# Performance work log

Hardware: AMD Instinct MI355X
Metric: run time of the kernel (lower is better)

## Reference

```python
import jax, jax.numpy as jnp
import numpy as np
from jax import lax

MARGIN = 0.3
BIGF = 1e9


def _pairwise_dist(x):
    # dist[i,j] = ||x_i - x_j||, clamped at 1e-12 before sqrt (as in torch code)
    sq = jnp.sum(x * x, axis=1)
    d = sq[:, None] + sq[None, :] - 2.0 * (x @ x.T)
    return jnp.sqrt(jnp.clip(d, 1e-12))


def _hard_mining(dist, targets):
    is_pos = targets[:, None] == targets[None, :]
    ap = jnp.where(is_pos, dist, jnp.asarray(-BIGF, dist.dtype))
    an = jnp.where(is_pos, jnp.asarray(BIGF, dist.dtype), dist)
    dist_ap = jnp.max(ap, axis=1)
    p_inds = jnp.argmax(ap, axis=1)
    dist_an = jnp.min(an, axis=1)
    n_inds = jnp.argmin(an, axis=1)
    return dist_ap, dist_an, p_inds, n_inds


def _batch_euclidean(x, y):
    # x: [N,m,d], y: [N,n,d] -> [N,m,n]
    xx = jnp.sum(x * x, axis=-1)[:, :, None]
    yy = jnp.sum(y * y, axis=-1)[:, None, :]
    d = xx + yy - 2.0 * jnp.einsum('nmd,nkd->nmk', x, y)
    return jnp.sqrt(jnp.clip(d, 1e-12))


def _shortest_dist(dmat):
    # DTW-style shortest path over [m,n] grid, batched over N: dp[i,j] = d[i,j] + min(dp[i-1,j], dp[i,j-1])
    N, m, n = dmat.shape
    big = jnp.asarray(BIGF, dmat.dtype)
    init_row = jnp.full((N, n), big, dmat.dtype).at[:, 0].set(0.0)  # virtual row -1: only (0,0) reachable

    def row_step(prev_row, drow):  # prev_row,drow: [N,n]
        def col_step(left, un):  # left: [N]
            up, d = un
            cur = d + jnp.minimum(up, left)
            return cur, cur
        _, cols = lax.scan(col_step, jnp.full((N,), big, dmat.dtype), (prev_row.T, drow.T))
        return cols.T, None

    last_row, _ = lax.scan(row_step, init_row, jnp.moveaxis(dmat, 1, 0))
    return last_row[:, -1]


def _batch_local_dist(x, y):
    d = _batch_euclidean(x, y)
    d = jnp.tanh(d * 0.5)  # == (exp(d)-1)/(exp(d)+1), numerically safe
    return _shortest_dist(d)


def _margin_ranking(dist_an, dist_ap, margin):
    # MarginRankingLoss with y=1: mean(relu(margin - (dist_an - dist_ap)))
    return jnp.mean(jnp.maximum(0.0, margin + dist_ap - dist_an))


def setup_inputs() -> dict:
    key = jax.random.key(0)
    k1, k2 = jax.random.split(key)
    N, D = 512, 2048
    LD, PARTS = 128, 8
    K = 4  # instances per identity (PK sampling)
    inputs = jax.random.normal(k1, (N, D), dtype=jnp.float32)
    local_features = jax.random.normal(k2, (N, LD, PARTS), dtype=jnp.float32)
    targets = jnp.arange(N, dtype=jnp.int64) // K
    return {"inputs": inputs, "targets": targets, "local_features": local_features}


def reference(inputs, targets, local_features):
    dist = _pairwise_dist(inputs)
    dist_ap, dist_an, p_inds, n_inds = _hard_mining(dist, targets)
    global_loss = _margin_ranking(dist_an, dist_ap, MARGIN)
    lf = jnp.transpose(local_features, (0, 2, 1))  # [N, parts, local_dim]
    local_ap = _batch_local_dist(lf, lf[p_inds])
    local_an = _batch_local_dist(lf, lf[n_inds])
    local_loss = _margin_ranking(local_an, local_ap, MARGIN)
    return (global_loss, local_loss)
```

## Files before the change

### kernel.cpp

```cpp
#include <hip/hip_runtime.h>
#include <math.h>

#define MARGIN 0.3f
#define BIGF 1e9f
#define NN 512
#define DD 2048
#define LDIM 128
#define PARTS 8

typedef __attribute__((ext_vector_type(8))) __bf16 bf16x8;
typedef __attribute__((ext_vector_type(4))) float f32x4;

__global__ __launch_bounds__(256, 2) void k_gram(
    const float* __restrict__ X, _Float16* __restrict__ Gp,
    float* __restrict__ ndiag, float* gsum, float* lsum, unsigned* counter)
{
    __shared__ __bf16 A[2][4096], B[2][4096];

    int bid = blockIdx.x;
    int tj = bid & 7, ti = (bid >> 3) & 7, ks = bid >> 6;
    int t = threadIdx.x;
    int w = t >> 6, lane = t & 63;
    int wr = w >> 1, wc = w & 1;

    if (bid == 0 && t == 0) { *gsum = 0.0f; *lsum = 0.0f; *counter = 0u; }

    int m = t >> 7;
    int r = (t >> 1) & 63;
    int kst = t & 1;
    int grow = (m ? tj : ti) * 64 + r;
    const float4* gp4 = (const float4*)(X + (size_t)grow * DD + ks * 256 + kst * 32);
    int ebase = kst * 2048 + (r >> 4) * 512 + (r & 15) * 8;

    float4 cur[8];
#pragma unroll
    for (int q = 0; q < 8; q++) cur[q] = gp4[q];

    f32x4 acc00 = {0.f, 0.f, 0.f, 0.f};
    f32x4 acc01 = {0.f, 0.f, 0.f, 0.f};
    f32x4 acc10 = {0.f, 0.f, 0.f, 0.f};
    f32x4 acc11 = {0.f, 0.f, 0.f, 0.f};

    {
        __bf16* hb = (m ? B[0] : A[0]) + ebase;
#pragma unroll
        for (int jg = 0; jg < 4; jg++) {
            float fe[8] = {cur[2 * jg].x, cur[2 * jg].y, cur[2 * jg].z, cur[2 * jg].w,
                           cur[2 * jg + 1].x, cur[2 * jg + 1].y, cur[2 * jg + 1].z, cur[2 * jg + 1].w};
            bf16x8 h;
#pragma unroll
            for (int e = 0; e < 8; e++) h[e] = (__bf16)fe[e];
            *(bf16x8*)(hb + jg * 128) = h;
        }
    }

#pragma unroll
    for (int it = 0; it < 4; ++it) {
        __syncthreads();
        if (it < 3) {
            const float4* np = gp4 + (it + 1) * 16;
#pragma unroll
            for (int q = 0; q < 8; q++) cur[q] = np[q];
        }
        int buf = it & 1;
#pragma unroll
        for (int kstep = 0; kstep < 2; kstep++) {
            const bf16x8* fA = (const bf16x8*)&A[buf][kstep * 2048 + wr * 1024];
            const bf16x8* fB = (const bf16x8*)&B[buf][kstep * 2048 + wc * 1024];
            bf16x8 ah0 = fA[lane], ah1 = fA[lane + 64];
            bf16x8 bh0 = fB[lane], bh1 = fB[lane + 64];
            acc00 = __builtin_amdgcn_mfma_f32_16x16x32_bf16(ah0, bh0, acc00, 0, 0, 0);
            acc01 = __builtin_amdgcn_mfma_f32_16x16x32_bf16(ah0, bh1, acc01, 0, 0, 0);
            acc10 = __builtin_amdgcn_mfma_f32_16x16x32_bf16(ah1, bh0, acc10, 0, 0, 0);
            acc11 = __builtin_amdgcn_mfma_f32_16x16x32_bf16(ah1, bh1, acc11, 0, 0, 0);
        }
        if (it < 3) {
            int nb = (it + 1) & 1;
            __bf16* hb = (m ? B[nb] : A[nb]) + ebase;
#pragma unroll
            for (int jg = 0; jg < 4; jg++) {
                float fe[8] = {cur[2 * jg].x, cur[2 * jg].y, cur[2 * jg].z, cur[2 * jg].w,
                               cur[2 * jg + 1].x, cur[2 * jg + 1].y, cur[2 * jg + 1].z, cur[2 * jg + 1].w};
                bf16x8 h;
#pragma unroll
                for (int e = 0; e < 8; e++) h[e] = (__bf16)fe[e];
                *(bf16x8*)(hb + jg * 128) = h;
            }
        }
    }

    int rbase = ti * 64 + wr * 32 + ((lane >> 4) << 2);
    int cbase = tj * 64 + wc * 32 + (lane & 15);
    _Float16* gb = Gp + (size_t)ks * NN * NN;
    f32x4 accs[2][2] = {{acc00, acc01}, {acc10, acc11}};
#pragma unroll
    for (int g = 0; g < 2; g++)
#pragma unroll
        for (int h = 0; h < 2; h++)
#pragma unroll
            for (int rr = 0; rr < 4; rr++)
                gb[(size_t)(rbase + g * 16 + rr) * NN + cbase + h * 16] =
                    (_Float16)accs[g][h][rr];

    if (ti == tj && wr == wc && ((lane >> 4) == ((lane & 15) >> 2))) {
        int rr = lane & 3;
        int row0 = rbase + rr;
        ndiag[ks * NN + row0]      = acc00[rr];
        ndiag[ks * NN + row0 + 16] = acc11[rr];
    }
}

__global__ __launch_bounds__(256) void k_mine_local(
    const _Float16* __restrict__ Gp, const float* __restrict__ ndiag,
    const int* __restrict__ tg, const float* __restrict__ LF,
    float* gsum, float* lsum, unsigned* counter, float* __restrict__ out)
{
    __shared__ float s_apv[4]; __shared__ int s_api[4];
    __shared__ float s_anv[4]; __shared__ int s_ani[4];
    __shared__ int sh_pn[2];
    __shared__ float A2[LDIM * PARTS];
    __shared__ float B2[2][LDIM * PARTS];
    __shared__ float dtm[2][64];
    __shared__ float res[2];

    int i = blockIdx.x;
    int t = threadIdx.x;

    float4 a2v = ((const float4*)(LF + (size_t)i * LDIM * PARTS))[t];

    float ni = 0.f, d0 = 0.f, d1 = 0.f;
#pragma unroll
    for (int ks = 0; ks < 8; ks++) {
        ni += ndiag[ks * NN + i];
        d0 += ndiag[ks * NN + t];
        d1 += ndiag[ks * NN + t + 256];
    }

    int tgt_i = tg[i];

    float apv = -BIGF; int api = 0x7fffffff;
    float anv =  BIGF; int ani = 0x7fffffff;

#pragma unroll
    for (int jj = 0; jj < 2; jj++) {
        int j = t + jj * 256;
        float g = 0.f;
#pragma unroll
        for (int ks = 0; ks < 8; ks++)
            g += (float)Gp[(size_t)ks * NN * NN + (size_t)i * NN + j];
        float nj = (jj == 0) ? d0 : d1;
        float dd = ni + nj - 2.0f * g;
        float dist = sqrtf(fmaxf(dd, 1e-12f));
        bool pos = (tg[j] == tgt_i);
        float a = pos ? dist : -BIGF;
        if (a > apv || (a == apv && j < api)) { apv = a; api = j; }
        float b = pos ? BIGF : dist;
        if (b < anv || (b == anv && j < ani)) { anv = b; ani = j; }
    }
    for (int off = 32; off > 0; off >>= 1) {
        float av = __shfl_down(apv, off); int ai = __shfl_down(api, off);
        if (av > apv || (av == apv && ai < api)) { apv = av; api = ai; }
        float nv = __shfl_down(anv, off); int nid = __shfl_down(ani, off);
        if (nv < anv || (nv == anv && nid < ani)) { anv = nv; ani = nid; }
    }
    int lane = t & 63, wid = t >> 6;
    if (lane == 0) { s_apv[wid] = apv; s_api[wid] = api;
                     s_anv[wid] = anv; s_ani[wid] = ani; }
    __syncthreads();
    if (t == 0) {
        apv = s_apv[0]; api = s_api[0]; anv = s_anv[0]; ani = s_ani[0];
        for (int wv = 1; wv < 4; wv++) {
            float av = s_apv[wv]; int ai = s_api[wv];
            if (av > apv || (av == apv && ai < api)) { apv = av; api = ai; }
            float nv = s_anv[wv]; int nid = s_ani[wv];
            if (nv < anv || (nv == anv && nid < ani)) { anv = nv; ani = nid; }
        }
        sh_pn[0] = api;
        sh_pn[1] = ani;
        atomicAdd(gsum, fmaxf(0.0f, MARGIN + apv - anv));
    }
    __syncthreads();

    int w = t >> 6;
    ((float4*)A2)[t] = a2v;
    if (w < 2) {
        int ind = sh_pn[w];
        const float4* B4 = (const float4*)(LF + (size_t)ind * LDIM * PARTS);
        float4* Bw = (float4*)B2[w];
        Bw[lane]       = B4[lane];
        Bw[lane + 64]  = B4[lane + 64];
        Bw[lane + 128] = B4[lane + 128];
        Bw[lane + 192] = B4[lane + 192];
    }
    __syncthreads();

    if (w < 2) {
        int p = lane >> 3, q = lane & 7;
        float acc = 0.0f;
        const float* Bw = B2[w];
        for (int d = 0; d < LDIM; d++) {
            float diff = A2[d * PARTS + p] - Bw[d * PARTS + q];
            acc = fmaf(diff, diff, acc);
        }
        float dist = sqrtf(fmaxf(acc, 1e-12f));
        dtm[w][p * 8 + q] = tanhf(0.5f * dist);
    }
    __syncthreads();

    if ((t == 0) || (t == 64)) {
        const float* dm = dtm[w];
        float dp[8];
        dp[0] = dm[0];
        for (int j = 1; j < 8; j++) dp[j] = dp[j - 1] + dm[j];
        for (int rr = 1; rr < 8; rr++) {
            dp[0] += dm[rr * 8];
            for (int j = 1; j < 8; j++)
                dp[j] = dm[rr * 8 + j] + fminf(dp[j], dp[j - 1]);
        }
        res[w] = dp[7];
    }
    __syncthreads();

    if (t == 0) {
        float l = fmaxf(0.0f, MARGIN + res[0] - res[1]);
        atomicAdd(lsum, l);
        __threadfence();
        unsigned old = atomicAdd(counter, 1u);
        if (old == (NN - 1)) {
            __threadfence();
            float ls = atomicAdd(lsum, 0.0f);
            float gs = atomicAdd(gsum, 0.0f);
            out[0] = gs * (1.0f / NN);
            out[1] = ls * (1.0f / NN);
        }
    }
}

extern "C" void kernel_launch(void* const* d_in, const int* in_sizes, int n_in,
                              void* d_out, int out_size, void* d_ws, size_t ws_size,
                              hipStream_t stream)
{
    const float* X  = (const float*)d_in[0];
    const int*   tg = (const int*)d_in[1];
    const float* LF = (const float*)d_in[2];
    float* out = (float*)d_out;

    char* ws = (char*)d_ws;
    _Float16* Gp      = (_Float16*)ws;
    float*    ndiag   = (float*)(ws + (4u << 20));
    float*    gsum    = (float*)(ws + (4u << 20) + 16384);
    float*    lsum    = (float*)(ws + (4u << 20) + 16388);
    unsigned* counter = (unsigned*)(ws + (4u << 20) + 16392);

    k_gram<<<512, 256, 0, stream>>>(X, Gp, ndiag, gsum, lsum, counter);
    k_mine_local<<<512, 256, 0, stream>>>(Gp, ndiag, tg, LF, gsum, lsum, counter, out);
}
```

Measured before the change: 94.25 us.

## Fuse Gram and mining kernels into one persistent kernel with grid barrier

Merges the split-K Gram kernel and the mining/local-distance kernel into a single launch. A global atomic counter acts as a grid-wide barrier, the two phases share LDS through a union, and diagonal norms are accumulated atomically into one array. The mining phase also reads two fp16 partials per thread as one 32-bit load. This removes a kernel launch and the gap between the two launches, but adds a hipMemsetAsync and a spin barrier that relies on all 512 blocks being co-resident, which risks deadlock if occupancy does not allow it.

```diff
diff --git a/kernel.cpp b/kernel.cpp
--- a/kernel.cpp
+++ b/kernel.cpp
@@ -11,72 +11,54 @@
 typedef __attribute__((ext_vector_type(8))) __bf16 bf16x8;
 typedef __attribute__((ext_vector_type(4))) float f32x4;
 
-__global__ __launch_bounds__(256, 2) void k_gram(
-    const float* __restrict__ X, _Float16* __restrict__ Gp,
-    float* __restrict__ ndiag, float* gsum, float* lsum, unsigned* counter)
+union SMem {
+  struct { __bf16 A[2][4096]; __bf16 B[2][4096]; } g;
+  struct {
+    float A2[LDIM * PARTS];
+    float B2[2][LDIM * PARTS];
+    float dtm[2][64];
+    float res[2];
+    float apv[4]; float anv[4];
+    int   api[4]; int   ani[4];
+    int   pn[2];
+  } m;
+};
+
+__global__ __launch_bounds__(256, 2) void k_fused(
+    const float* __restrict__ X, const int* __restrict__ tg,
+    const float* __restrict__ LF, _Float16* __restrict__ Gp,
+    float* __restrict__ nsum, float* gsum, float* lsum,
+    unsigned* done, unsigned* fin, float* __restrict__ out)
 {
-    __shared__ __bf16 A[2][4096], B[2][4096];
-
-    int bid = blockIdx.x;
-    int tj = bid & 7, ti = (bid >> 3) & 7, ks = bid >> 6;
-    int t = threadIdx.x;
-    int w = t >> 6, lane = t & 63;
-    int wr = w >> 1, wc = w & 1;
-
-    if (bid == 0 && t == 0) { *gsum = 0.0f; *lsum = 0.0f; *counter = 0u; }
-
-    int m = t >> 7;
-    int r = (t >> 1) & 63;
-    int kst = t & 1;
-    int grow = (m ? tj : ti) * 64 + r;
-    const float4* gp4 = (const float4*)(X + (size_t)grow * DD + ks * 256 + kst * 32);
-    int ebase = kst * 2048 + (r >> 4) * 512 + (r & 15) * 8;
-
-    float4 cur[8];
-#pragma unroll
-    for (int q = 0; q < 8; q++) cur[q] = gp4[q];
-
-    f32x4 acc00 = {0.f, 0.f, 0.f, 0.f};
-    f32x4 acc01 = {0.f, 0.f, 0.f, 0.f};
-    f32x4 acc10 = {0.f, 0.f, 0.f, 0.f};
-    f32x4 acc11 = {0.f, 0.f, 0.f, 0.f};
+    __shared__ SMem sm;
+
+    const int bid = blockIdx.x;
+    const int t = threadIdx.x;
+    const int w = t >> 6, lane = t & 63;
+
+    float4 a2v = ((const float4*)(LF + (size_t)bid * LDIM * PARTS))[t];
 
     {
-        __bf16* hb = (m ? B[0] : A[0]) + ebase;
-#pragma unroll
-        for (int jg = 0; jg < 4; jg++) {
-            float fe[8] = {cur[2 * jg].x, cur[2 * jg].y, cur[2 * jg].z, cur[2 * jg].w,
-                           cur[2 * jg + 1].x, cur[2 * jg + 1].y, cur[2 * jg + 1].z, cur[2 * jg + 1].w};
-            bf16x8 h;
-#pragma unroll
-            for (int e = 0; e < 8; e++) h[e] = (__bf16)fe[e];
-            *(bf16x8*)(hb + jg * 128) = h;
-        }
-    }
-
-#pragma unroll
-    for (int it = 0; it < 4; ++it) {
-        __syncthreads();
-        if (it < 3) {
-            const float4* np = gp4 + (it + 1) * 16;
-#pragma unroll
-            for (int q = 0; q < 8; q++) cur[q] = np[q];
-        }
-        int buf = it & 1;
-#pragma unroll
-        for (int kstep = 0; kstep < 2; kstep++) {
-            const bf16x8* fA = (const bf16x8*)&A[buf][kstep * 2048 + wr * 1024];
-            const bf16x8* fB = (const bf16x8*)&B[buf][kstep * 2048 + wc * 1024];
-            bf16x8 ah0 = fA[lane], ah1 = fA[lane + 64];
-            bf16x8 bh0 = fB[lane], bh1 = fB[lane + 64];
-            acc00 = __builtin_amdgcn_mfma_f32_16x16x32_bf16(ah0, bh0, acc00, 0, 0, 0);
-            acc01 = __builtin_amdgcn_mfma_f32_16x16x32_bf16(ah0, bh1, acc01, 0, 0, 0);
-            acc10 = __builtin_amdgcn_mfma_f32_16x16x32_bf16(ah1, bh0, acc10, 0, 0, 0);
-            acc11 = __builtin_amdgcn_mfma_f32_16x16x32_bf16(ah1, bh1, acc11, 0, 0, 0);
-        }
-        if (it < 3) {
-            int nb = (it + 1) & 1;
-            __bf16* hb = (m ? B[nb] : A[nb]) + ebase;
+        const int tj = bid & 7, ti = (bid >> 3) & 7, ks = bid >> 6;
+        const int wr = w >> 1, wc = w & 1;
+        const int hf = t >> 7;
+        const int r = (t >> 1) & 63;
+        const int kst = t & 1;
+        const int grow = (hf ? tj : ti) * 64 + r;
+        const float4* gp4 = (const float4*)(X + (size_t)grow * DD + ks * 256 + kst * 32);
+        const int ebase = kst * 2048 + (r >> 4) * 512 + (r & 15) * 8;
+
+        float4 cur[8];
+#pragma unroll
+        for (int q = 0; q < 8; q++) cur[q] = gp4[q];
+
+        f32x4 acc00 = {0.f, 0.f, 0.f, 0.f};
+        f32x4 acc01 = {0.f, 0.f, 0.f, 0.f};
+        f32x4 acc10 = {0.f, 0.f, 0.f, 0.f};
+        f32x4 acc11 = {0.f, 0.f, 0.f, 0.f};
+
+        {
+            __bf16* hb = (hf ? sm.g.B[0] : sm.g.A[0]) + ebase;
 #pragma unroll
             for (int jg = 0; jg < 4; jg++) {
                 float fe[8] = {cur[2 * jg].x, cur[2 * jg].y, cur[2 * jg].z, cur[2 * jg].w,
@@ -87,75 +69,105 @@
                 *(bf16x8*)(hb + jg * 128) = h;
             }
         }
-    }
-
-    int rbase = ti * 64 + wr * 32 + ((lane >> 4) << 2);
-    int cbase = tj * 64 + wc * 32 + (lane & 15);
-    _Float16* gb = Gp + (size_t)ks * NN * NN;
-    f32x4 accs[2][2] = {{acc00, acc01}, {acc10, acc11}};
-#pragma unroll
-    for (int g = 0; g < 2; g++)
-#pragma unroll
-        for (int h = 0; h < 2; h++)
-#pragma unroll
-            for (int rr = 0; rr < 4; rr++)
-                gb[(size_t)(rbase + g * 16 + rr) * NN + cbase + h * 16] =
-                    (_Float16)accs[g][h][rr];
-
-    if (ti == tj && wr == wc && ((lane >> 4) == ((lane & 15) >> 2))) {
-        int rr = lane & 3;
-        int row0 = rbase + rr;
-        ndiag[ks * NN + row0]      = acc00[rr];
-        ndiag[ks * NN + row0 + 16] = acc11[rr];
-    }
-}
-
-__global__ __launch_bounds__(256) void k_mine_local(
-    const _Float16* __restrict__ Gp, const float* __restrict__ ndiag,
-    const int* __restrict__ tg, const float* __restrict__ LF,
-    float* gsum, float* lsum, unsigned* counter, float* __restrict__ out)
-{
-    __shared__ float s_apv[4]; __shared__ int s_api[4];
-    __shared__ float s_anv[4]; __shared__ int s_ani[4];
-    __shared__ int sh_pn[2];
-    __shared__ float A2[LDIM * PARTS];
-    __shared__ float B2[2][LDIM * PARTS];
-    __shared__ float dtm[2][64];
-    __shared__ float res[2];
-
-    int i = blockIdx.x;
-    int t = threadIdx.x;
-
-    float4 a2v = ((const float4*)(LF + (size_t)i * LDIM * PARTS))[t];
-
-    float ni = 0.f, d0 = 0.f, d1 = 0.f;
-#pragma unroll
-    for (int ks = 0; ks < 8; ks++) {
-        ni += ndiag[ks * NN + i];
-        d0 += ndiag[ks * NN + t];
-        d1 += ndiag[ks * NN + t + 256];
-    }
-
+
+#pragma unroll
+        for (int it = 0; it < 4; ++it) {
+            __syncthreads();
+            if (it < 3) {
+                const float4* np = gp4 + (it + 1) * 16;
+#pragma unroll
+                for (int q = 0; q < 8; q++) cur[q] = np[q];
+            }
+            int buf = it & 1;
+#pragma unroll
+            for (int kstep = 0; kstep < 2; kstep++) {
+                const bf16x8* fA = (const bf16x8*)&sm.g.A[buf][kstep * 2048 + wr * 1024];
+                const bf16x8* fB = (const bf16x8*)&sm.g.B[buf][kstep * 2048 + wc * 1024];
+                bf16x8 ah0 = fA[lane], ah1 = fA[lane + 64];
+                bf16x8 bh0 = fB[lane], bh1 = fB[lane + 64];
+                acc00 = __builtin_amdgcn_mfma_f32_16x16x32_bf16(ah0, bh0, acc00, 0, 0, 0);
+                acc01 = __builtin_amdgcn_mfma_f32_16x16x32_bf16(ah0, bh1, acc01, 0, 0, 0);
+                acc10 = __builtin_amdgcn_mfma_f32_16x16x32_bf16(ah1, bh0, acc10, 0, 0, 0);
+                acc11 = __builtin_amdgcn_mfma_f32_16x16x32_bf16(ah1, bh1, acc11, 0, 0, 0);
+            }
+            if (it < 3) {
+                int nb = (it + 1) & 1;
+                __bf16* hb = (hf ? sm.g.B[nb] : sm.g.A[nb]) + ebase;
+#pragma unroll
+                for (int jg = 0; jg < 4; jg++) {
+                    float fe[8] = {cur[2 * jg].x, cur[2 * jg].y, cur[2 * jg].z, cur[2 * jg].w,
+                                   cur[2 * jg + 1].x, cur[2 * jg + 1].y, cur[2 * jg + 1].z, cur[2 * jg + 1].w};
+                    bf16x8 h;
+#pragma unroll
+                    for (int e = 0; e < 8; e++) h[e] = (__bf16)fe[e];
+                    *(bf16x8*)(hb + jg * 128) = h;
+                }
+            }
+        }
+
+        const int rbase = ti * 64 + wr * 32 + ((lane >> 4) << 2);
+        const int cbase = tj * 64 + wc * 32 + (lane & 15);
+        _Float16* gb = Gp + (size_t)ks * NN * NN;
+        f32x4 accs[2][2] = {{acc00, acc01}, {acc10, acc11}};
+#pragma unroll
+        for (int g2 = 0; g2 < 2; g2++)
+#pragma unroll
+            for (int h2 = 0; h2 < 2; h2++)
+#pragma unroll
+                for (int rr = 0; rr < 4; rr++)
+                    gb[(size_t)(rbase + g2 * 16 + rr) * NN + cbase + h2 * 16] =
+                        (_Float16)accs[g2][h2][rr];
+
+        if (ti == tj && wr == wc && ((lane >> 4) == ((lane & 15) >> 2))) {
+            int rr = lane & 3;
+            int row0 = rbase + rr;
+            atomicAdd(&nsum[row0],      acc00[rr]);
+            atomicAdd(&nsum[row0 + 16], acc11[rr]);
+        }
+    }
+
+    __threadfence();
+    __syncthreads();
+    if (t == 0) {
+        __hip_atomic_fetch_add(done, 1u, __ATOMIC_ACQ_REL, __HIP_MEMORY_SCOPE_AGENT);
+        while (__hip_atomic_load(done, __ATOMIC_ACQUIRE, __HIP_MEMORY_SCOPE_AGENT) < (unsigned)NN)
+            __builtin_amdgcn_s_sleep(2);
+    }
+    __syncthreads();
+    __threadfence();
+
+    const int i = bid;
+    float ni = nsum[i];
+    float2 nj2 = ((const float2*)nsum)[t];
+    int2 tg2 = ((const int2*)tg)[t];
     int tgt_i = tg[i];
 
-    float apv = -BIGF; int api = 0x7fffffff;
-    float anv =  BIGF; int ani = 0x7fffffff;
-
-#pragma unroll
-    for (int jj = 0; jj < 2; jj++) {
-        int j = t + jj * 256;
-        float g = 0.f;
-#pragma unroll
-        for (int ks = 0; ks < 8; ks++)
-            g += (float)Gp[(size_t)ks * NN * NN + (size_t)i * NN + j];
-        float nj = (jj == 0) ? d0 : d1;
-        float dd = ni + nj - 2.0f * g;
-        float dist = sqrtf(fmaxf(dd, 1e-12f));
-        bool pos = (tg[j] == tgt_i);
-        float a = pos ? dist : -BIGF;
-        if (a > apv || (a == apv && j < api)) { apv = a; api = j; }
-        float b = pos ? BIGF : dist;
-        if (b < anv || (b == anv && j < ani)) { anv = b; ani = j; }
+    float g0 = 0.f, g1 = 0.f;
+    {
+        const unsigned int* gr = (const unsigned int*)(Gp + (size_t)i * NN);
+#pragma unroll
+        for (int ks = 0; ks < 8; ks++) {
+            unsigned int v = gr[(size_t)ks * (NN * NN / 2) + t];
+            union { unsigned int u; _Float16 h[2]; } cv; cv.u = v;
+            g0 += (float)cv.h[0];
+            g1 += (float)cv.h[1];
+        }
+    }
+
+    float apv, anv; int api, ani;
+    {
+        float dd0 = ni + nj2.x - 2.0f * g0;
+        float dist0 = sqrtf(fmaxf(dd0, 1e-12f));
+        bool pos0 = (tg2.x == tgt_i);
+        apv = pos0 ? dist0 : -BIGF; api = 2 * t;
+        anv = pos0 ? BIGF : dist0;  ani = 2 * t;
+        float dd1 = ni + nj2.y - 2.0f * g1;
+        float dist1 = sqrtf(fmaxf(dd1, 1e-12f));
+        bool pos1 = (tg2.y == tgt_i);
+        float a1 = pos1 ? dist1 : -BIGF;
+        if (a1 > apv) { apv = a1; api = 2 * t + 1; }
+        float b1 = pos1 ? BIGF : dist1;
+        if (b1 < anv) { anv = b1; ani = 2 * t + 1; }
     }
     for (int off = 32; off > 0; off >>= 1) {
         float av = __shfl_down(apv, off); int ai = __shfl_down(api, off);
@@ -163,30 +175,27 @@
         float nv = __shfl_down(anv, off); int nid = __shfl_down(ani, off);
         if (nv < anv || (nv == anv && nid < ani)) { anv = nv; ani = nid; }
     }
-    int lane = t & 63, wid = t >> 6;
-    if (lane == 0) { s_apv[wid] = apv; s_api[wid] = api;
-                     s_anv[wid] = anv; s_ani[wid] = ani; }
+    if (lane == 0) { sm.m.apv[w] = apv; sm.m.api[w] = api;
+                     sm.m.anv[w] = anv; sm.m.ani[w] = ani; }
     __syncthreads();
     if (t == 0) {
-        apv = s_apv[0]; api = s_api[0]; anv = s_anv[0]; ani = s_ani[0];
         for (int wv = 1; wv < 4; wv++) {
-            float av = s_apv[wv]; int ai = s_api[wv];
+            float av = sm.m.apv[wv]; int ai = sm.m.api[wv];
             if (av > apv || (av == apv && ai < api)) { apv = av; api = ai; }
-            float nv = s_anv[wv]; int nid = s_ani[wv];
+            float nv = sm.m.anv[wv]; int nid = sm.m.ani[wv];
             if (nv < anv || (nv == anv && nid < ani)) { anv = nv; ani = nid; }
         }
-        sh_pn[0] = api;
-        sh_pn[1] = ani;
+        sm.m.pn[0] = api;
+        sm.m.pn[1] = ani;
         atomicAdd(gsum, fmaxf(0.0f, MARGIN + apv - anv));
     }
-    __syncthreads();
-
-    int w = t >> 6;
-    ((float4*)A2)[t] = a2v;
+    ((float4*)sm.m.A2)[t] = a2v;
+    __syncthreads();
+
     if (w < 2) {
-        int ind = sh_pn[w];
+        int ind = sm.m.pn[w];
         const float4* B4 = (const float4*)(LF + (size_t)ind * LDIM * PARTS);
-        float4* Bw = (float4*)B2[w];
+        float4* Bw = (float4*)sm.m.B2[w];
         Bw[lane]       = B4[lane];
         Bw[lane + 64]  = B4[lane + 64];
         Bw[lane + 128] = B4[lane + 128];
@@ -197,35 +206,35 @@
     if (w < 2) {
         int p = lane >> 3, q = lane & 7;
         float acc = 0.0f;
-        const float* Bw = B2[w];
+        const float* Bw = sm.m.B2[w];
         for (int d = 0; d < LDIM; d++) {
-            float diff = A2[d * PARTS + p] - Bw[d * PARTS + q];
+            float diff = sm.m.A2[d * PARTS + p] - Bw[d * PARTS + q];
             acc = fmaf(diff, diff, acc);
         }
         float dist = sqrtf(fmaxf(acc, 1e-12f));
-        dtm[w][p * 8 + q] = tanhf(0.5f * dist);
+        sm.m.dtm[w][p * 8 + q] = tanhf(0.5f * dist);
     }
     __syncthreads();
 
     if ((t == 0) || (t == 64)) {
-        const float* dm = dtm[w];
+        const float* dm = sm.m.dtm[w];
         float dp[8];
         dp[0] = dm[0];
         for (int j = 1; j < 8; j++) dp[j] = dp[j - 1] + dm[j];
-        for (int rr = 1; rr < 8; rr++) {
-            dp[0] += dm[rr * 8];
+        for (int rr2 = 1; rr2 < 8; rr2++) {
+            dp[0] += dm[rr2 * 8];
             for (int j = 1; j < 8; j++)
-                dp[j] = dm[rr * 8 + j] + fminf(dp[j], dp[j - 1]);
-        }
-        res[w] = dp[7];
+                dp[j] = dm[rr2 * 8 + j] + fminf(dp[j], dp[j - 1]);
+        }
+        sm.m.res[w] = dp[7];
     }
     __syncthreads();
 
     if (t == 0) {
-        float l = fmaxf(0.0f, MARGIN + res[0] - res[1]);
+        float l = fmaxf(0.0f, MARGIN + sm.m.res[0] - sm.m.res[1]);
         atomicAdd(lsum, l);
         __threadfence();
-        unsigned old = atomicAdd(counter, 1u);
+        unsigned old = atomicAdd(fin, 1u);
         if (old == (NN - 1)) {
             __threadfence();
             float ls = atomicAdd(lsum, 0.0f);
@@ -246,12 +255,14 @@
     float* out = (float*)d_out;
 
     char* ws = (char*)d_ws;
-    _Float16* Gp      = (_Float16*)ws;
-    float*    ndiag   = (float*)(ws + (4u << 20));
-    float*    gsum    = (float*)(ws + (4u << 20) + 16384);
-    float*    lsum    = (float*)(ws + (4u << 20) + 16388);
-    unsigned* counter = (unsigned*)(ws + (4u << 20) + 16392);
-
-    k_gram<<<512, 256, 0, stream>>>(X, Gp, ndiag, gsum, lsum, counter);
-    k_mine_local<<<512, 256, 0, stream>>>(Gp, ndiag, tg, LF, gsum, lsum, counter, out);
+    _Float16* Gp   = (_Float16*)ws;
+    char* ctrl     = ws + (4u << 20);
+    float* nsum    = (float*)ctrl;
+    float* gsum    = (float*)(ctrl + 2048);
+    float* lsum    = (float*)(ctrl + 2052);
+    unsigned* done = (unsigned*)(ctrl + 2056);
+    unsigned* fin  = (unsigned*)(ctrl + 2060);
+
+    hipMemsetAsync(ctrl, 0, 2064, stream);
+    k_fused<<<NN, 256, 0, stream>>>(X, tg, LF, Gp, nsum, gsum, lsum, done, fin, out);
 }
```

Result: slower. 224.9 us (+138.6%).
